# Kernel tuning notes

Measured on AMD Instinct MI355X. Metric: run time of the kernel, lower is better.

The kernel has to match this reference:

```python
import jax, jax.numpy as jnp
import numpy as np

LLR_CLIP = 20.0
BIG = 1e30


def _pam_gray(b):
    if len(b) > 1:
        return (1 - 2 * b[0]) * (2 ** len(b[1:]) - _pam_gray(b[1:]))
    return 1 - 2 * b[0]


def _qam_points(nbps):
    ns = 2 ** nbps
    pts = np.zeros(ns, np.complex64)
    for i in range(ns):
        b = np.array([int(c) for c in np.binary_repr(i, nbps)])
        pts[i] = _pam_gray(b[0::2]) + 1j * _pam_gray(b[1::2])
    nh = nbps // 2
    qam_var = 1.0 / (2 ** (nh - 2)) * sum((2 * j + 1) ** 2 for j in range(2 ** (nh - 1)))
    return (pts / np.sqrt(qam_var)).astype(np.complex64)


def setup_inputs() -> dict:
    B, M, S = 8192, 16, 8
    nbps = 4
    ns = 2 ** nbps
    rng = np.random.default_rng(0)
    points = _qam_points(nbps)
    h = ((rng.standard_normal((B, M, S)) + 1j * rng.standard_normal((B, M, S))) / np.sqrt(2 * S)).astype(np.complex64)
    idx = rng.integers(0, ns, (B, S))
    x = points[idx]
    no = 0.05
    A = (rng.standard_normal((B, M, M)) + 1j * rng.standard_normal((B, M, M))) / np.sqrt(2 * M)
    s = no * (np.eye(M)[None] + 0.5 * A @ np.conj(np.swapaxes(A, -1, -2)))
    s = 0.5 * (s + np.conj(np.swapaxes(s, -1, -2)))  # exact Hermitian PSD noise covariance
    L = np.linalg.cholesky(s)
    w = (rng.standard_normal((B, M)) + 1j * rng.standard_normal((B, M))) / np.sqrt(2)
    n = np.einsum('bmn,bn->bm', L, w)
    y = np.einsum('bms,bs->bm', h, x) + n
    return {
        'y_re': jnp.asarray(y.real, jnp.float32), 'y_im': jnp.asarray(y.imag, jnp.float32),
        'h_re': jnp.asarray(h.real, jnp.float32), 'h_im': jnp.asarray(h.imag, jnp.float32),
        's_re': jnp.asarray(s.real, jnp.float32), 's_im': jnp.asarray(s.imag, jnp.float32),
        'points_re': jnp.asarray(points.real, jnp.float32), 'points_im': jnp.asarray(points.imag, jnp.float32),
        'k': 64,
    }


def _kbest_llrs(y, h, s, points, k):
    B, M = y.shape
    S = h.shape[-1]
    ns = points.shape[0]
    nbps = int(round(np.log2(ns)))
    # --- whitening: s^{-1/2} via Hermitian eigendecomposition ---
    e, U = jnp.linalg.eigh(s)
    s_isqrt = (U * (1.0 / jnp.sqrt(e))[:, None, :]) @ jnp.conj(jnp.swapaxes(U, -1, -2))
    yw = jnp.einsum('bmn,bn->bm', s_isqrt, y)
    hw = jnp.einsum('bmn,bns->bms', s_isqrt, h)
    # --- sort columns by norm (descending), QR, premultiply by Q^H ---
    norms = jnp.sum(jnp.abs(hw) ** 2, axis=1)            # [B,S]
    perm = jnp.argsort(-norms, axis=-1)                  # [B,S]
    hs = jnp.take_along_axis(hw, perm[:, None, :], axis=2)
    Q, R = jnp.linalg.qr(hs)                             # Q:[B,M,S], R:[B,S,S]
    ybar = jnp.einsum('bms,bm->bs', jnp.conj(Q), yw)     # [B,S] complex
    # --- K-best tree search over streams i = S-1 .. 0 ---
    dists0 = jnp.broadcast_to(jnp.where(jnp.arange(k) == 0, 0.0, BIG).astype(jnp.float32), (B, k))
    syms0 = jnp.zeros((B, k, S), jnp.int32)

    def step(carry, i):
        dists, syms = carry
        r_row = R[:, i, :]                               # [B,S]
        mask = jnp.arange(S) > i                         # already-detected streams
        xsel = points[syms]                              # [B,k,S]
        partial = jnp.sum(jnp.where(mask, r_row[:, None, :] * xsel, 0.0), axis=-1)  # [B,k]
        rii = r_row[:, i]                                # [B]
        resid = ybar[:, i][:, None, None] - partial[:, :, None] - rii[:, None, None] * points[None, None, :]
        cand = dists[:, :, None] + jnp.abs(resid) ** 2   # [B,k,ns]
        neg, idx = jax.lax.top_k(-cand.reshape(B, k * ns), k)
        parent = idx // ns
        new_sym = (idx % ns).astype(jnp.int32)
        syms = jnp.take_along_axis(syms, parent[:, :, None], axis=1)
        syms = jnp.where(jnp.arange(S)[None, None, :] == i, new_sym[:, :, None], syms)
        return (-neg, syms), None

    (dists, syms), _ = jax.lax.scan(step, (dists0, syms0), jnp.arange(S - 1, -1, -1))
    # --- unsort streams back to original order ---
    inv = jnp.argsort(perm, axis=-1)
    syms = jnp.take_along_axis(syms, inv[:, None, :], axis=2)  # [B,k,S]
    # --- List2LLRSimple: min-distance hypotheses per bit ---
    bits = (jnp.arange(ns)[:, None] >> jnp.arange(nbps - 1, -1, -1)[None, :]) & 1  # [ns,nb]
    cb = bits[syms]                                      # [B,k,S,nb]
    d = dists[:, :, None, None]
    d0 = jnp.min(jnp.where(cb == 0, d, BIG), axis=1)     # [B,S,nb]
    d1 = jnp.min(jnp.where(cb == 1, d, BIG), axis=1)
    return jnp.clip(d0 - d1, -LLR_CLIP, LLR_CLIP)        # LLR = ln P(b=1)/P(b=0)


def reference(y_re, y_im, h_re, h_im, s_re, s_im, points_re, points_im, k):
    y = y_re + 1j * y_im
    h = h_re + 1j * h_im
    s = s_re + 1j * s_im
    points = points_re + 1j * points_im
    return _kbest_llrs(y, h, s, points, int(k))
```

## Files before the change

kernel.cpp:

```cpp
#include <hip/hip_runtime.h>


#define BIGF 1e30f
#define CLIPV 20.0f

__device__ __forceinline__ void tri_decode(int t, int &a, int &b) {
    int a0 = (int)((sqrtf(8.0f * (float)t + 1.0f) - 1.0f) * 0.5f);
    while ((a0 + 1) * (a0 + 2) / 2 <= t) ++a0;
    while ((a0 * (a0 + 1)) / 2 > t) --a0;
    a = a0;
    b = t - (a0 * (a0 + 1)) / 2;
}

__global__ __launch_bounds__(64) void kbest16_kernel(
    const float* __restrict__ y_re, const float* __restrict__ y_im,
    const float* __restrict__ h_re, const float* __restrict__ h_im,
    const float* __restrict__ s_re, const float* __restrict__ s_im,
    const float* __restrict__ p_re, const float* __restrict__ p_im,
    float* __restrict__ out)
{
    __shared__ double A[16][16][2];
    __shared__ double W[16][9][2];
    __shared__ double G[8][8][2];
    __shared__ double bv[8][2];
    __shared__ double nrm[8];
    __shared__ float Rm[8][8][2];
    __shared__ float yb[8][2];
    __shared__ float pts[16][2];
    __shared__ float rp[16][2];
    __shared__ float sel_d[64];
    __shared__ unsigned sel_s[64];
    __shared__ int perm[8];
    __shared__ int invp[8];

    const int lane = threadIdx.x;
    const int b = blockIdx.x;

    const float* sre = s_re + (size_t)b * 256;
    const float* simm = s_im + (size_t)b * 256;
    const float* hre = h_re + (size_t)b * 128;
    const float* him = h_im + (size_t)b * 128;

    #pragma unroll
    for (int t = 0; t < 4; ++t) {
        int e = lane + 64 * t;
        A[e >> 4][e & 15][0] = (double)sre[e];
        A[e >> 4][e & 15][1] = (double)simm[e];
    }
    #pragma unroll
    for (int t = 0; t < 2; ++t) {
        int e = lane + 64 * t;
        W[e >> 3][e & 7][0] = (double)hre[e];
        W[e >> 3][e & 7][1] = (double)him[e];
    }
    if (lane < 16) {
        W[lane][8][0] = (double)y_re[(size_t)b * 16 + lane];
        W[lane][8][1] = (double)y_im[(size_t)b * 16 + lane];
        pts[lane][0] = p_re[lane];
        pts[lane][1] = p_im[lane];
    }
    __syncthreads();

    for (int j = 0; j < 16; ++j) {
        double djj = sqrt(A[j][j][0]);
        double inv = 1.0 / djj;
        __syncthreads();
        if (lane == 0) A[j][j][0] = djj;
        int i = j + 1 + lane;
        if (i < 16) { A[i][j][0] *= inv; A[i][j][1] *= inv; }
        __syncthreads();
        int n = 15 - j, tot = (n * (n + 1)) / 2;
        for (int t = lane; t < tot; t += 64) {
            int a, c; tri_decode(t, a, c);
            int ii = j + 1 + a, kk = j + 1 + c;
            double lir = A[ii][j][0], lii = A[ii][j][1];
            double lkr = A[kk][j][0], lki = A[kk][j][1];
            A[ii][kk][0] -= lir * lkr + lii * lki;
            A[ii][kk][1] -= lii * lkr - lir * lki;
        }
        __syncthreads();
    }

    for (int r = 0; r < 16; ++r) {
        double inv = 1.0 / A[r][r][0];
        if (lane < 9) { W[r][lane][0] *= inv; W[r][lane][1] *= inv; }
        __syncthreads();
        int rem = (15 - r) * 9;
        for (int t = lane; t < rem; t += 64) {
            int i = r + 1 + t / 9, c = t % 9;
            double lr = A[i][r][0], li = A[i][r][1];
            double wr = W[r][c][0], wi = W[r][c][1];
            W[i][c][0] -= lr * wr - li * wi;
            W[i][c][1] -= lr * wi + li * wr;
        }
        __syncthreads();
    }

    if (lane < 8) {
        double s = 0.0;
        #pragma unroll
        for (int m = 0; m < 16; ++m)
            s += W[m][lane][0] * W[m][lane][0] + W[m][lane][1] * W[m][lane][1];
        nrm[lane] = s;
    }
    __syncthreads();
    if (lane < 8) {
        double ni = nrm[lane];
        int rank = 0;
        #pragma unroll
        for (int jj = 0; jj < 8; ++jj) {
            double nj = nrm[jj];
            rank += (nj > ni || (nj == ni && jj < lane)) ? 1 : 0;
        }
        perm[rank] = lane;
        invp[lane] = rank;
    }
    __syncthreads();

    if (lane < 44) {
        int a, c;
        int isG = lane < 36;
        if (isG) tri_decode(lane, a, c); else { a = lane - 36; c = 0; }
        int pa = perm[a];
        int pc = isG ? perm[c] : 8;
        double ar = 0.0, ai = 0.0;
        #pragma unroll
        for (int m = 0; m < 16; ++m) {
            double xr = W[m][pa][0], xi = W[m][pa][1];
            double yr = W[m][pc][0], yi = W[m][pc][1];
            ar += xr * yr + xi * yi;
            ai += xr * yi - xi * yr;
        }
        if (isG) { G[a][c][0] = ar; G[a][c][1] = ai; }
        else { bv[a][0] = ar; bv[a][1] = ai; }
    }
    __syncthreads();

    for (int j = 0; j < 8; ++j) {
        double djj = sqrt(G[j][j][0]);
        double inv = 1.0 / djj;
        __syncthreads();
        if (lane == 0) G[j][j][0] = djj;
        int i = j + 1 + lane;
        if (i < 8) { G[i][j][0] *= inv; G[i][j][1] *= inv; }
        __syncthreads();
        int n = 7 - j, tot = (n * (n + 1)) / 2;
        if (lane < tot) {
            int a, c; tri_decode(lane, a, c);
            int ii = j + 1 + a, kk = j + 1 + c;
            double lir = G[ii][j][0], lii = G[ii][j][1];
            double lkr = G[kk][j][0], lki = G[kk][j][1];
            G[ii][kk][0] -= lir * lkr + lii * lki;
            G[ii][kk][1] -= lii * lkr - lir * lki;
        }
        __syncthreads();
    }
    if (lane < 36) {
        int a, c; tri_decode(lane, a, c);
        Rm[c][a][0] = (float)G[a][c][0];
        Rm[c][a][1] = (float)(-G[a][c][1]);
    }

    for (int r = 0; r < 8; ++r) {
        if (lane == 0) {
            double inv = 1.0 / G[r][r][0];
            bv[r][0] *= inv; bv[r][1] *= inv;
        }
        __syncthreads();
        int i = r + 1 + lane;
        if (i < 8) {
            double lr = G[i][r][0], li = G[i][r][1];
            double wr = bv[r][0], wi = bv[r][1];
            bv[i][0] -= lr * wr - li * wi;
            bv[i][1] -= lr * wi + li * wr;
        }
        __syncthreads();
    }
    if (lane < 8) { yb[lane][0] = (float)bv[lane][0]; yb[lane][1] = (float)bv[lane][1]; }
    __syncthreads();

    float dist; unsigned syms;
    if (lane < 16) {
        float r77 = Rm[7][7][0];
        float er = yb[7][0] - r77 * pts[lane][0];
        float ei = yb[7][1] - r77 * pts[lane][1];
        dist = er * er + ei * ei;
        syms = (unsigned)lane << 28;
    } else {
        dist = BIGF;
        syms = 0u;
    }

    for (int lev = 6; lev >= 0; --lev) {
        __syncthreads();
        if (lane < 16) {
            float rii = Rm[lev][lev][0];
            rp[lane][0] = rii * pts[lane][0];
            rp[lane][1] = rii * pts[lane][1];
        }
        __syncthreads();

        float pr = 0.0f, pi = 0.0f;
        for (int j = lev + 1; j < 8; ++j) {
            int sj = (syms >> (4 * j)) & 15;
            float xr = pts[sj][0], xi = pts[sj][1];
            float rr = Rm[lev][j][0], ri = Rm[lev][j][1];
            pr += rr * xr - ri * xi;
            pi += rr * xi + ri * xr;
        }
        float tr = yb[lev][0] - pr, ti = yb[lev][1] - pi;

        float d[16];
        #pragma unroll
        for (int p = 0; p < 16; ++p) {
            float er = tr - rp[p][0], ei = ti - rp[p][1];
            d[p] = dist + (er * er + ei * ei);
        }

        float mnl = d[0];
        #pragma unroll
        for (int p = 1; p < 16; ++p) mnl = fminf(mnl, d[p]);
        float gmn = mnl, gmx = mnl;
        #pragma unroll
        for (int off = 32; off > 0; off >>= 1) {
            gmn = fminf(gmn, __shfl_xor(gmn, off));
            gmx = fmaxf(gmx, __shfl_xor(gmx, off));
        }
        unsigned lo = __float_as_uint(gmn) + 1u;
        unsigned hi = __float_as_uint(gmx) + 1u;
        bool exact = false;
        unsigned Bb = 0u;
        while (lo < hi) {
            unsigned mid = (lo + hi) >> 1;
            float Tf = __uint_as_float(mid);
            int c = 0;
            #pragma unroll
            for (int p = 0; p < 16; ++p) c += (d[p] < Tf) ? 1 : 0;
            #pragma unroll
            for (int off = 32; off > 0; off >>= 1) c += __shfl_xor(c, off);
            if (c == 64) { Bb = mid; exact = true; break; }
            if (c > 64) hi = mid; else lo = mid + 1u;
        }
        float Tlt, Teq;
        if (exact) { Tlt = __uint_as_float(Bb); Teq = -1.0f; }
        else       { Tlt = __uint_as_float(lo - 1u); Teq = Tlt; }

        int cl = 0, ce = 0;
        #pragma unroll
        for (int p = 0; p < 16; ++p) {
            cl += (d[p] < Tlt) ? 1 : 0;
            ce += (d[p] == Teq) ? 1 : 0;
        }
        int v = cl | (ce << 16);
        int sc = v;
        #pragma unroll
        for (int off = 1; off < 64; off <<= 1) {
            int t = __shfl_up(sc, off);
            if (lane >= off) sc += t;
        }
        int excl = sc - v;
        int tots = __shfl(sc, 63);
        int offL = excl & 0xffff;
        int offE = excl >> 16;
        int totL = tots & 0xffff;

        unsigned base = syms & ~(15u << (4 * lev));
        int slot = offL;
        #pragma unroll
        for (int p = 0; p < 16; ++p) {
            if (d[p] < Tlt) {
                sel_d[slot] = d[p];
                sel_s[slot] = base | ((unsigned)p << (4 * lev));
                ++slot;
            }
        }
        int eslot = totL + offE;
        #pragma unroll
        for (int p = 0; p < 16; ++p) {
            if (d[p] == Teq) {
                if (eslot < 64) {
                    sel_d[eslot] = d[p];
                    sel_s[eslot] = base | ((unsigned)p << (4 * lev));
                }
                ++eslot;
            }
        }
        __syncthreads();
        dist = sel_d[lane];
        syms = sel_s[lane];
    }
    __syncthreads();

    if (lane < 32) {
        int s = lane >> 2, jj = lane & 3;
        int sh = 4 * invp[s] + (3 - jj);
        float d0 = BIGF, d1 = BIGF;
        for (int c = 0; c < 64; ++c) {
            float dc = sel_d[c];
            unsigned cs = sel_s[c];
            if ((cs >> sh) & 1u) d1 = fminf(d1, dc);
            else d0 = fminf(d0, dc);
        }
        float llr = d0 - d1;
        llr = fminf(fmaxf(llr, -CLIPV), CLIPV);
        out[(size_t)b * 32 + lane] = llr;
    }
}

extern "C" void kernel_launch(void* const* d_in, const int* in_sizes, int n_in,
                              void* d_out, int out_size, void* d_ws, size_t ws_size,
                              hipStream_t stream) {
    (void)n_in; (void)d_ws; (void)ws_size; (void)out_size;
    const float* y_re = (const float*)d_in[0];
    const float* y_im = (const float*)d_in[1];
    const float* h_re = (const float*)d_in[2];
    const float* h_im = (const float*)d_in[3];
    const float* s_re = (const float*)d_in[4];
    const float* s_im = (const float*)d_in[5];
    const float* p_re = (const float*)d_in[6];
    const float* p_im = (const float*)d_in[7];
    int B = in_sizes[0] / 16;
    kbest16_kernel<<<dim3(B), dim3(64), 0, stream>>>(
        y_re, y_im, h_re, h_im, s_re, s_im, p_re, p_im, (float*)d_out);
}
```

Measured before the change: 293.5 us.

## Pack four wave-independent problems per block with wave-level sync and ballot scans

```diff
diff --git a/kernel.cpp b/kernel.cpp
--- a/kernel.cpp
+++ b/kernel.cpp
@@ -3,6 +3,10 @@
 
 #define BIGF 1e30f
 #define CLIPV 20.0f
+#define WPB 4
+#define WAVE_DBL 864
+
+#define WSYNC() asm volatile("s_waitcnt lgkmcnt(0)" ::: "memory")
 
 __device__ __forceinline__ void tri_decode(int t, int &a, int &b) {
     int a0 = (int)((sqrtf(8.0f * (float)t + 1.0f) - 1.0f) * 0.5f);
@@ -12,32 +16,39 @@
     b = t - (a0 * (a0 + 1)) / 2;
 }
 
-__global__ __launch_bounds__(64) void kbest16_kernel(
+__device__ __forceinline__ int mbcnt64(unsigned long long m) {
+    int r = __builtin_amdgcn_mbcnt_lo((unsigned)m, 0);
+    return __builtin_amdgcn_mbcnt_hi((unsigned)(m >> 32), r);
+}
+
+__global__ __launch_bounds__(256, 5) void kbest16_kernel(
     const float* __restrict__ y_re, const float* __restrict__ y_im,
     const float* __restrict__ h_re, const float* __restrict__ h_im,
     const float* __restrict__ s_re, const float* __restrict__ s_im,
     const float* __restrict__ p_re, const float* __restrict__ p_im,
     float* __restrict__ out)
 {
-    __shared__ double A[16][16][2];
-    __shared__ double W[16][9][2];
-    __shared__ double G[8][8][2];
-    __shared__ double bv[8][2];
-    __shared__ double nrm[8];
-    __shared__ float Rm[8][8][2];
-    __shared__ float yb[8][2];
-    __shared__ float pts[16][2];
-    __shared__ float rp[16][2];
-    __shared__ float sel_d[64];
-    __shared__ unsigned sel_s[64];
-    __shared__ int perm[8];
-    __shared__ int invp[8];
-
-    const int lane = threadIdx.x;
-    const int b = blockIdx.x;
+    __shared__ double smem[WPB * WAVE_DBL];
+
+    const int tid = threadIdx.x;
+    const int wid = tid >> 6;
+    const int lane = tid & 63;
+    const int b = blockIdx.x * WPB + wid;
+
+    double* wb = &smem[(size_t)wid * WAVE_DBL];
+    double (*A)[17][2]  = (double(*)[17][2])wb;
+    double (*Wm)[10][2] = (double(*)[10][2])(wb + 544);
+    double (*G)[9][2] = (double(*)[9][2])wb;
+    double (*bv)[2]   = (double(*)[2])(wb + 144);
+    double* nrm       = wb + 160;
+    int* perm         = (int*)(wb + 168);
+    int* invp         = (int*)(wb + 172);
+    float (*Rm)[9][2] = (float(*)[9][2])(wb + 176);
+    float (*yb)[2]    = (float(*)[2])(wb + 248);
+    unsigned long long* sel = (unsigned long long*)(wb + 256);
 
     const float* sre = s_re + (size_t)b * 256;
-    const float* simm = s_im + (size_t)b * 256;
+    const float* sim = s_im + (size_t)b * 256;
     const float* hre = h_re + (size_t)b * 128;
     const float* him = h_im + (size_t)b * 128;
 
@@ -45,30 +56,29 @@
     for (int t = 0; t < 4; ++t) {
         int e = lane + 64 * t;
         A[e >> 4][e & 15][0] = (double)sre[e];
-        A[e >> 4][e & 15][1] = (double)simm[e];
+        A[e >> 4][e & 15][1] = (double)sim[e];
     }
     #pragma unroll
     for (int t = 0; t < 2; ++t) {
         int e = lane + 64 * t;
-        W[e >> 3][e & 7][0] = (double)hre[e];
-        W[e >> 3][e & 7][1] = (double)him[e];
+        Wm[e >> 3][e & 7][0] = (double)hre[e];
+        Wm[e >> 3][e & 7][1] = (double)him[e];
     }
     if (lane < 16) {
-        W[lane][8][0] = (double)y_re[(size_t)b * 16 + lane];
-        W[lane][8][1] = (double)y_im[(size_t)b * 16 + lane];
-        pts[lane][0] = p_re[lane];
-        pts[lane][1] = p_im[lane];
-    }
-    __syncthreads();
+        Wm[lane][8][0] = (double)y_re[(size_t)b * 16 + lane];
+        Wm[lane][8][1] = (double)y_im[(size_t)b * 16 + lane];
+    }
+    float plr = p_re[lane & 15];
+    float pli = p_im[lane & 15];
+    WSYNC();
 
     for (int j = 0; j < 16; ++j) {
         double djj = sqrt(A[j][j][0]);
         double inv = 1.0 / djj;
-        __syncthreads();
         if (lane == 0) A[j][j][0] = djj;
         int i = j + 1 + lane;
         if (i < 16) { A[i][j][0] *= inv; A[i][j][1] *= inv; }
-        __syncthreads();
+        WSYNC();
         int n = 15 - j, tot = (n * (n + 1)) / 2;
         for (int t = lane; t < tot; t += 64) {
             int a, c; tri_decode(t, a, c);
@@ -78,32 +88,32 @@
             A[ii][kk][0] -= lir * lkr + lii * lki;
             A[ii][kk][1] -= lii * lkr - lir * lki;
         }
-        __syncthreads();
+        WSYNC();
     }
 
     for (int r = 0; r < 16; ++r) {
         double inv = 1.0 / A[r][r][0];
-        if (lane < 9) { W[r][lane][0] *= inv; W[r][lane][1] *= inv; }
-        __syncthreads();
+        if (lane < 9) { Wm[r][lane][0] *= inv; Wm[r][lane][1] *= inv; }
+        WSYNC();
         int rem = (15 - r) * 9;
         for (int t = lane; t < rem; t += 64) {
             int i = r + 1 + t / 9, c = t % 9;
             double lr = A[i][r][0], li = A[i][r][1];
-            double wr = W[r][c][0], wi = W[r][c][1];
-            W[i][c][0] -= lr * wr - li * wi;
-            W[i][c][1] -= lr * wi + li * wr;
-        }
-        __syncthreads();
+            double wr = Wm[r][c][0], wi = Wm[r][c][1];
+            Wm[i][c][0] -= lr * wr - li * wi;
+            Wm[i][c][1] -= lr * wi + li * wr;
+        }
+        WSYNC();
     }
 
     if (lane < 8) {
         double s = 0.0;
         #pragma unroll
         for (int m = 0; m < 16; ++m)
-            s += W[m][lane][0] * W[m][lane][0] + W[m][lane][1] * W[m][lane][1];
+            s += Wm[m][lane][0] * Wm[m][lane][0] + Wm[m][lane][1] * Wm[m][lane][1];
         nrm[lane] = s;
     }
-    __syncthreads();
+    WSYNC();
     if (lane < 8) {
         double ni = nrm[lane];
         int rank = 0;
@@ -115,7 +125,7 @@
         perm[rank] = lane;
         invp[lane] = rank;
     }
-    __syncthreads();
+    WSYNC();
 
     if (lane < 44) {
         int a, c;
@@ -126,24 +136,23 @@
         double ar = 0.0, ai = 0.0;
         #pragma unroll
         for (int m = 0; m < 16; ++m) {
-            double xr = W[m][pa][0], xi = W[m][pa][1];
-            double yr = W[m][pc][0], yi = W[m][pc][1];
+            double xr = Wm[m][pa][0], xi = Wm[m][pa][1];
+            double yr = Wm[m][pc][0], yi = Wm[m][pc][1];
             ar += xr * yr + xi * yi;
             ai += xr * yi - xi * yr;
         }
         if (isG) { G[a][c][0] = ar; G[a][c][1] = ai; }
         else { bv[a][0] = ar; bv[a][1] = ai; }
     }
-    __syncthreads();
+    WSYNC();
 
     for (int j = 0; j < 8; ++j) {
         double djj = sqrt(G[j][j][0]);
         double inv = 1.0 / djj;
-        __syncthreads();
         if (lane == 0) G[j][j][0] = djj;
         int i = j + 1 + lane;
         if (i < 8) { G[i][j][0] *= inv; G[i][j][1] *= inv; }
-        __syncthreads();
+        WSYNC();
         int n = 7 - j, tot = (n * (n + 1)) / 2;
         if (lane < tot) {
             int a, c; tri_decode(lane, a, c);
@@ -153,20 +162,19 @@
             G[ii][kk][0] -= lir * lkr + lii * lki;
             G[ii][kk][1] -= lii * lkr - lir * lki;
         }
-        __syncthreads();
+        WSYNC();
     }
     if (lane < 36) {
         int a, c; tri_decode(lane, a, c);
         Rm[c][a][0] = (float)G[a][c][0];
         Rm[c][a][1] = (float)(-G[a][c][1]);
     }
-
     for (int r = 0; r < 8; ++r) {
         if (lane == 0) {
             double inv = 1.0 / G[r][r][0];
             bv[r][0] *= inv; bv[r][1] *= inv;
         }
-        __syncthreads();
+        WSYNC();
         int i = r + 1 + lane;
         if (i < 8) {
             double lr = G[i][r][0], li = G[i][r][1];
@@ -174,46 +182,39 @@
             bv[i][0] -= lr * wr - li * wi;
             bv[i][1] -= lr * wi + li * wr;
         }
-        __syncthreads();
+        WSYNC();
     }
     if (lane < 8) { yb[lane][0] = (float)bv[lane][0]; yb[lane][1] = (float)bv[lane][1]; }
-    __syncthreads();
+    WSYNC();
 
     float dist; unsigned syms;
-    if (lane < 16) {
+    {
         float r77 = Rm[7][7][0];
-        float er = yb[7][0] - r77 * pts[lane][0];
-        float ei = yb[7][1] - r77 * pts[lane][1];
-        dist = er * er + ei * ei;
-        syms = (unsigned)lane << 28;
-    } else {
-        dist = BIGF;
-        syms = 0u;
+        float er = yb[7][0] - r77 * p_re[lane & 15];
+        float ei = yb[7][1] - r77 * p_im[lane & 15];
+        float dr = er * er + ei * ei;
+        dist = (lane < 16) ? dr : BIGF;
+        syms = (lane < 16) ? ((unsigned)lane << 28) : 0u;
     }
 
     for (int lev = 6; lev >= 0; --lev) {
-        __syncthreads();
-        if (lane < 16) {
-            float rii = Rm[lev][lev][0];
-            rp[lane][0] = rii * pts[lane][0];
-            rp[lane][1] = rii * pts[lane][1];
-        }
-        __syncthreads();
-
-        float pr = 0.0f, pi = 0.0f;
+        float pr = 0.0f, pim = 0.0f;
         for (int j = lev + 1; j < 8; ++j) {
             int sj = (syms >> (4 * j)) & 15;
-            float xr = pts[sj][0], xi = pts[sj][1];
+            float xr = __shfl(plr, sj);
+            float xi = __shfl(pli, sj);
             float rr = Rm[lev][j][0], ri = Rm[lev][j][1];
             pr += rr * xr - ri * xi;
-            pi += rr * xi + ri * xr;
-        }
-        float tr = yb[lev][0] - pr, ti = yb[lev][1] - pi;
+            pim += rr * xi + ri * xr;
+        }
+        float rii = Rm[lev][lev][0];
+        float tr = yb[lev][0] - pr, ti = yb[lev][1] - pim;
 
         float d[16];
         #pragma unroll
         for (int p = 0; p < 16; ++p) {
-            float er = tr - rp[p][0], ei = ti - rp[p][1];
+            float er = tr - rii * p_re[p];
+            float ei = ti - rii * p_im[p];
             d[p] = dist + (er * er + ei * ei);
         }
 
@@ -235,9 +236,8 @@
             float Tf = __uint_as_float(mid);
             int c = 0;
             #pragma unroll
-            for (int p = 0; p < 16; ++p) c += (d[p] < Tf) ? 1 : 0;
-            #pragma unroll
-            for (int off = 32; off > 0; off >>= 1) c += __shfl_xor(c, off);
+            for (int p = 0; p < 16; ++p)
+                c += __popcll(__ballot(d[p] < Tf));
             if (c == 64) { Bb = mid; exact = true; break; }
             if (c > 64) hi = mid; else lo = mid + 1u;
         }
@@ -245,32 +245,22 @@
         if (exact) { Tlt = __uint_as_float(Bb); Teq = -1.0f; }
         else       { Tlt = __uint_as_float(lo - 1u); Teq = Tlt; }
 
-        int cl = 0, ce = 0;
+        int offL = 0, offE = 0, totL = 0;
         #pragma unroll
         for (int p = 0; p < 16; ++p) {
-            cl += (d[p] < Tlt) ? 1 : 0;
-            ce += (d[p] == Teq) ? 1 : 0;
-        }
-        int v = cl | (ce << 16);
-        int sc = v;
-        #pragma unroll
-        for (int off = 1; off < 64; off <<= 1) {
-            int t = __shfl_up(sc, off);
-            if (lane >= off) sc += t;
-        }
-        int excl = sc - v;
-        int tots = __shfl(sc, 63);
-        int offL = excl & 0xffff;
-        int offE = excl >> 16;
-        int totL = tots & 0xffff;
-
+            unsigned long long mlt = __ballot(d[p] < Tlt);
+            unsigned long long meq = __ballot(d[p] == Teq);
+            offL += mbcnt64(mlt);
+            offE += mbcnt64(meq);
+            totL += __popcll(mlt);
+        }
         unsigned base = syms & ~(15u << (4 * lev));
         int slot = offL;
         #pragma unroll
         for (int p = 0; p < 16; ++p) {
             if (d[p] < Tlt) {
-                sel_d[slot] = d[p];
-                sel_s[slot] = base | ((unsigned)p << (4 * lev));
+                unsigned ns = base | ((unsigned)p << (4 * lev));
+                sel[slot] = ((unsigned long long)ns << 32) | (unsigned long long)__float_as_uint(d[p]);
                 ++slot;
             }
         }
@@ -279,28 +269,35 @@
         for (int p = 0; p < 16; ++p) {
             if (d[p] == Teq) {
                 if (eslot < 64) {
-                    sel_d[eslot] = d[p];
-                    sel_s[eslot] = base | ((unsigned)p << (4 * lev));
+                    unsigned ns = base | ((unsigned)p << (4 * lev));
+                    sel[eslot] = ((unsigned long long)ns << 32) | (unsigned long long)__float_as_uint(d[p]);
                 }
                 ++eslot;
             }
         }
-        __syncthreads();
-        dist = sel_d[lane];
-        syms = sel_s[lane];
-    }
-    __syncthreads();
+        WSYNC();
+        unsigned long long v = sel[lane];
+        dist = __uint_as_float((unsigned)v);
+        syms = (unsigned)(v >> 32);
+    }
 
     if (lane < 32) {
         int s = lane >> 2, jj = lane & 3;
-        int sh = 4 * invp[s] + (3 - jj);
-        float d0 = BIGF, d1 = BIGF;
-        for (int c = 0; c < 64; ++c) {
-            float dc = sel_d[c];
-            unsigned cs = sel_s[c];
-            if ((cs >> sh) & 1u) d1 = fminf(d1, dc);
-            else d0 = fminf(d0, dc);
-        }
+        int sh = 4 * invp[s] + (3 - jj) + 32;
+        float d0a = BIGF, d0b = BIGF, d1a = BIGF, d1b = BIGF;
+        for (int c = 0; c < 64; c += 2) {
+            unsigned long long v1 = sel[c];
+            unsigned long long v2 = sel[c + 1];
+            float f1 = __uint_as_float((unsigned)v1);
+            float f2 = __uint_as_float((unsigned)v2);
+            bool b1 = (v1 >> sh) & 1ull;
+            bool b2 = (v2 >> sh) & 1ull;
+            d1a = fminf(d1a, b1 ? f1 : BIGF);
+            d0a = fminf(d0a, b1 ? BIGF : f1);
+            d1b = fminf(d1b, b2 ? f2 : BIGF);
+            d0b = fminf(d0b, b2 ? BIGF : f2);
+        }
+        float d0 = fminf(d0a, d0b), d1 = fminf(d1a, d1b);
         float llr = d0 - d1;
         llr = fminf(fmaxf(llr, -CLIPV), CLIPV);
         out[(size_t)b * 32 + lane] = llr;
@@ -320,6 +317,6 @@
     const float* p_re = (const float*)d_in[6];
     const float* p_im = (const float*)d_in[7];
     int B = in_sizes[0] / 16;
-    kbest16_kernel<<<dim3(B), dim3(64), 0, stream>>>(
+    kbest16_kernel<<<dim3(B / WPB), dim3(64 * WPB), 0, stream>>>(
         y_re, y_im, h_re, h_im, s_re, s_im, p_re, p_im, (float*)d_out);
 }
```

Result: faster. 240.7 us (-18.0%).
